# Performance work log

Measured on AMD Instinct MI355X. Metric: run time of the kernel, lower is better.

## Reference

```python
import jax, jax.numpy as jnp
import numpy as np


def setup_inputs() -> dict:
    key = jax.random.key(0)
    ks = jax.random.split(key, 5)
    B, IN, OUT = 8192, 4096, 4096
    in_q, out_q = IN // 4, OUT // 4
    # xavier-uniform-like scale for weights
    lim = float(np.sqrt(6.0 / (in_q + out_q)))
    return {
        "x": jax.random.normal(ks[0], (B, IN), dtype=jnp.float32),
        "Wa": jax.random.uniform(ks[1], (in_q, out_q), jnp.float32, -lim, lim),
        "Wb": jax.random.uniform(ks[2], (in_q, out_q), jnp.float32, -lim, lim),
        "Wc": jax.random.uniform(ks[3], (in_q, out_q), jnp.float32, -lim, lim),
        "Wd": jax.random.uniform(ks[4], (in_q, out_q), jnp.float32, -lim, lim),
        "bias": jnp.zeros((OUT,), dtype=jnp.float32),
    }


def reference(x, Wa, Wb, Wc, Wd, bias):
    # split quaternion components: [B, in_q] each
    a, b, c, d = jnp.split(x, 4, axis=1)
    # Hamilton product with weight quaternion (right multiplication)
    out_a = a @ Wa - b @ Wb - c @ Wc - d @ Wd
    out_b = a @ Wb + b @ Wa + c @ Wd - d @ Wc
    out_c = a @ Wc - b @ Wd + c @ Wa + d @ Wb
    out_d = a @ Wd + b @ Wc - c @ Wb + d @ Wa
    return jnp.concatenate([out_a, out_b, out_c, out_d], axis=1) + bias
```

## Files before the change

kernel.cpp:

```cpp
#include <hip/hip_runtime.h>
#include <hip/hip_bf16.h>
#include <cstdint>
#include <cstddef>

typedef __bf16 bf16_t;
typedef __bf16 bf16x4 __attribute__((ext_vector_type(4)));
typedef __bf16 bf16x8 __attribute__((ext_vector_type(8)));
typedef float f32x4 __attribute__((ext_vector_type(4)));

#define GLD16(src, dst)                                                       \
    __builtin_amdgcn_global_load_lds(                                         \
        (const __attribute__((address_space(1))) void*)(src),                 \
        (__attribute__((address_space(3))) void*)(dst), 16, 0, 0)

#define BAR() asm volatile("s_barrier" ::: "memory")
#define WAIT_VM4() asm volatile("s_waitcnt vmcnt(4)" ::: "memory")
#define WAIT_VM6() asm volatile("s_waitcnt vmcnt(6)" ::: "memory")
#define WAIT_VM0() asm volatile("s_waitcnt vmcnt(0)" ::: "memory")

__global__ __launch_bounds__(256) void cvt_x_kernel(const float* __restrict__ x,
                                                    bf16_t* __restrict__ xb, int n4) {
    int idx = blockIdx.x * blockDim.x + threadIdx.x;
    int stride = gridDim.x * blockDim.x;
    const f32x4* xv = (const f32x4*)x;
    bf16x4* ov = (bf16x4*)xb;
    for (int i = idx; i < n4; i += stride) {
        f32x4 v = xv[i];
        bf16x4 o;
        o[0] = (bf16_t)v[0];
        o[1] = (bf16_t)v[1];
        o[2] = (bf16_t)v[2];
        o[3] = (bf16_t)v[3];
        ov[i] = o;
    }
}

__global__ __launch_bounds__(256) void pack_w_kernel(const float* __restrict__ Wa,
                                                     const float* __restrict__ Wb,
                                                     const float* __restrict__ Wc,
                                                     const float* __restrict__ Wd,
                                                     bf16_t* __restrict__ Mt) {
    __shared__ float tile[64][65];
    const int kb = blockIdx.x * 64;
    const int nb = blockIdx.y * 64;
    const int i = kb >> 10;
    const int j = nb >> 10;

    const float* W[4] = {Wa, Wb, Wc, Wd};
    const int srcIdx[4][4] = {{0, 1, 2, 3}, {1, 0, 3, 2}, {2, 3, 0, 1}, {3, 2, 1, 0}};
    const float sgn[4][4] = {{1.f, 1.f, 1.f, 1.f},
                             {-1.f, 1.f, -1.f, 1.f},
                             {-1.f, 1.f, 1.f, -1.f},
                             {-1.f, -1.f, 1.f, 1.f}};
    const float* Ws = W[srcIdx[i][j]];
    const float s = sgn[i][j];

    const int kq = kb & 1023;
    const int nq = nb & 1023;
    const int tx = threadIdx.x & 63;
    const int ty = threadIdx.x >> 6;

    for (int r = ty; r < 64; r += 4)
        tile[r][tx] = Ws[(size_t)(kq + r) * 1024 + (nq + tx)];
    __syncthreads();
    for (int r = ty; r < 64; r += 4)
        Mt[(size_t)(nb + r) * 4096 + (kb + tx)] = (bf16_t)(s * tile[tx][r]);
}

__global__ __launch_bounds__(512, 2) void qgemm_kernel(const bf16_t* __restrict__ A,
                                                       const bf16_t* __restrict__ Bt,
                                                       const float* __restrict__ bias,
                                                       float* __restrict__ C) {
    constexpr int N = 4096, K = 4096;
    constexpr int NT = K / 64;
    extern __shared__ __align__(16) char lds[];

    const int tid = threadIdx.x;
    const int w = tid >> 6;
    const int lane = tid & 63;
    const int l15 = lane & 15, l4 = lane >> 4;
    const int wr = w >> 2, wc = w & 3;

    const int wg = blockIdx.x;
    const int swz = (wg & 7) * 64 + (wg >> 3);
    const int brow = (swz >> 4) * 256;
    const int bcol = (swz & 15) * 256;

    const int srow = lane >> 3;
    const int skb = (lane & 7) ^ (lane >> 3);

    auto stageA = [&](int buf, int h, int tt) {
#pragma unroll
        for (int q = 0; q < 2; ++q) {
            const bf16_t* src = A + (size_t)(brow + h * 128 + w * 16 + q * 8 + srow) * K +
                                tt * 64 + skb * 8;
            GLD16(src, lds + buf * 32768 + h * 16384 + w * 2048 + q * 1024);
        }
    };
    auto stageB = [&](int buf, int h, int tt) {
#pragma unroll
        for (int q = 0; q < 2; ++q) {
            const bf16_t* src = Bt + (size_t)(bcol + h * 128 + w * 16 + q * 8 + srow) * K +
                                tt * 64 + skb * 8;
            GLD16(src, lds + 65536 + buf * 32768 + h * 16384 + w * 2048 + q * 1024);
        }
    };

    f32x4 acc[8][4] = {};
    bf16x8 a[4][2], b0[2][2], b1[2][2];

    auto ldAm = [&](int buf, int mh, int m) {
#pragma unroll
        for (int c = 0; c < 2; ++c)
            a[m][c] = *(const bf16x8*)(lds + buf * 32768 + wr * 16384 +
                                       (mh * 64 + m * 16 + l15) * 128 +
                                       ((c * 4 + l4) ^ (l15 & 7)) * 16);
    };
    auto ldB = [&](int buf, int nh, bf16x8(&b)[2][2]) {
#pragma unroll
        for (int n = 0; n < 2; ++n)
#pragma unroll
            for (int c = 0; c < 2; ++c)
                b[n][c] = *(const bf16x8*)(lds + 65536 + buf * 32768 + nh * 16384 +
                                           (wc * 32 + n * 16 + l15) * 128 +
                                           ((c * 4 + l4) ^ (l15 & 7)) * 16);
    };
    auto mmac = [&](int mh, int nh, bf16x8(&b)[2][2]) {
        __builtin_amdgcn_s_setprio(1);
#pragma unroll
        for (int m = 0; m < 4; ++m)
#pragma unroll
            for (int n = 0; n < 2; ++n)
#pragma unroll
                for (int c = 0; c < 2; ++c)
                    acc[mh * 4 + m][nh * 2 + n] = __builtin_amdgcn_mfma_f32_16x16x32_bf16(
                        a[m][c], b[n][c], acc[mh * 4 + m][nh * 2 + n], 0, 0, 0);
        __builtin_amdgcn_s_setprio(0);
    };

    stageA(0, 0, 0);
    stageA(0, 1, 0);
    stageB(0, 0, 0);
    stageB(0, 1, 0);
    stageB(1, 0, 1);
    stageB(1, 1, 1);
    stageA(1, 0, 1);
    WAIT_VM6();
    BAR();
    ldB(0, 0, b0);
    ldAm(0, 0, 0);
    ldAm(0, 0, 1);

    for (int tt = 0; tt < NT; ++tt) {
        const int cur = tt & 1;
        if (tt + 1 < NT) stageA(cur ^ 1, 1, tt + 1);
        BAR();
        ldAm(cur, 0, 2);
        ldAm(cur, 0, 3);
        mmac(0, 0, b0);
        ldB(cur, 1, b1);
        BAR();
        if (tt + 2 < NT) stageB(cur, 0, tt + 2);
        BAR();
        mmac(0, 1, b1);
        ldAm(cur, 1, 0);
        ldAm(cur, 1, 1);
        BAR();
        if (tt + 2 < NT) stageB(cur, 1, tt + 2);
        BAR();
        ldAm(cur, 1, 2);
        ldAm(cur, 1, 3);
        mmac(1, 1, b1);
        if (tt + 2 < NT) {
            WAIT_VM4();
        } else {
            WAIT_VM0();
        }
        BAR();
        if (tt + 2 < NT) stageA(cur, 0, tt + 2);
        BAR();
        mmac(1, 0, b0);
        if (tt + 1 < NT) {
            ldB(cur ^ 1, 0, b0);
            ldAm(cur ^ 1, 0, 0);
            ldAm(cur ^ 1, 0, 1);
        }
        BAR();
    }

#pragma unroll
    for (int n = 0; n < 4; ++n) {
        const int col = bcol + (n >> 1) * 128 + wc * 32 + (n & 1) * 16 + l15;
        const float bv = bias[col];
#pragma unroll
        for (int m = 0; m < 8; ++m) {
            const int row0 = brow + wr * 128 + m * 16 + l4 * 4;
            const f32x4 v = acc[m][n];
#pragma unroll
            for (int i = 0; i < 4; ++i)
                C[(size_t)(row0 + i) * N + col] = v[i] + bv;
        }
    }
}

extern "C" void kernel_launch(void* const* d_in, const int* in_sizes, int n_in,
                              void* d_out, int out_size, void* d_ws, size_t ws_size,
                              hipStream_t stream) {
    const float* x = (const float*)d_in[0];
    const float* Wa = (const float*)d_in[1];
    const float* Wb = (const float*)d_in[2];
    const float* Wc = (const float*)d_in[3];
    const float* Wd = (const float*)d_in[4];
    const float* bias = (const float*)d_in[5];
    float* out = (float*)d_out;

    const int M = 8192, N = 4096, K = 4096;

    bf16_t* xb = (bf16_t*)d_ws;
    bf16_t* Mt = xb + (size_t)M * K;

    cvt_x_kernel<<<4096, 256, 0, stream>>>(x, xb, (M * K) / 4);
    pack_w_kernel<<<dim3(64, 64), 256, 0, stream>>>(Wa, Wb, Wc, Wd, Mt);

    (void)hipFuncSetAttribute((const void*)qgemm_kernel,
                              hipFuncAttributeMaxDynamicSharedMemorySize, 131072);
    qgemm_kernel<<<dim3((M / 256) * (N / 256)), 512, 131072, stream>>>(xb, Mt, bias, out);
}
```

Measured before the change: 285.2 us.

## Switch GEMM inner loop from 16x16x32 to 32x32x16 bf16 MFMA tiles

Replaces the 16x16x32 MFMA micro-tiles with 32x32x16 MFMA, reorganising the accumulators into 32x32 f32x16 blocks and the LDS fragment loads into 32-row reads across four k-slices. Larger MFMA tiles cut the number of LDS fragment reads per FLOP and give higher per-instruction throughput. In exchange it changes the register layout, the swizzled LDS read pattern and the epilogue store mapping, which may alter register pressure and LDS bank-conflict behaviour.

```diff
diff --git a/kernel.cpp b/kernel.cpp
--- a/kernel.cpp
+++ b/kernel.cpp
@@ -7,6 +7,7 @@
 typedef __bf16 bf16x4 __attribute__((ext_vector_type(4)));
 typedef __bf16 bf16x8 __attribute__((ext_vector_type(8)));
 typedef float f32x4 __attribute__((ext_vector_type(4)));
+typedef float f32x16 __attribute__((ext_vector_type(16)));
 
 #define GLD16(src, dst)                                                       \
     __builtin_amdgcn_global_load_lds(                                         \
@@ -78,7 +79,7 @@
     const int tid = threadIdx.x;
     const int w = tid >> 6;
     const int lane = tid & 63;
-    const int l15 = lane & 15, l4 = lane >> 4;
+    const int l31 = lane & 31, l5 = lane >> 5;
     const int wr = w >> 2, wc = w & 3;
 
     const int wg = blockIdx.x;
@@ -106,35 +107,34 @@
         }
     };
 
-    f32x4 acc[8][4] = {};
-    bf16x8 a[4][2], b0[2][2], b1[2][2];
-
-    auto ldAm = [&](int buf, int mh, int m) {
-#pragma unroll
-        for (int c = 0; c < 2; ++c)
-            a[m][c] = *(const bf16x8*)(lds + buf * 32768 + wr * 16384 +
-                                       (mh * 64 + m * 16 + l15) * 128 +
-                                       ((c * 4 + l4) ^ (l15 & 7)) * 16);
-    };
-    auto ldB = [&](int buf, int nh, bf16x8(&b)[2][2]) {
-#pragma unroll
-        for (int n = 0; n < 2; ++n)
-#pragma unroll
-            for (int c = 0; c < 2; ++c)
-                b[n][c] = *(const bf16x8*)(lds + 65536 + buf * 32768 + nh * 16384 +
-                                           (wc * 32 + n * 16 + l15) * 128 +
-                                           ((c * 4 + l4) ^ (l15 & 7)) * 16);
-    };
-    auto mmac = [&](int mh, int nh, bf16x8(&b)[2][2]) {
+    f32x16 acc[4][2] = {};
+    bf16x8 a[2][4];
+    bf16x8 b0[4], b1[4];
+
+    auto ldA32 = [&](int buf, int mh, int m) {
+#pragma unroll
+        for (int ks = 0; ks < 4; ++ks) {
+            const int R = mh * 64 + m * 32 + l31;
+            a[m][ks] = *(const bf16x8*)(lds + buf * 32768 + wr * 16384 + R * 128 +
+                                        (((ks * 2 + l5) ^ (R & 7)) & 7) * 16);
+        }
+    };
+    auto ldB32 = [&](int buf, int nh, bf16x8(&b)[4]) {
+#pragma unroll
+        for (int ks = 0; ks < 4; ++ks) {
+            const int R = wc * 32 + l31;
+            b[ks] = *(const bf16x8*)(lds + 65536 + buf * 32768 + nh * 16384 + R * 128 +
+                                     (((ks * 2 + l5) ^ (R & 7)) & 7) * 16);
+        }
+    };
+    auto mmac = [&](int mh, int nh, bf16x8(&b)[4]) {
         __builtin_amdgcn_s_setprio(1);
 #pragma unroll
-        for (int m = 0; m < 4; ++m)
-#pragma unroll
-            for (int n = 0; n < 2; ++n)
-#pragma unroll
-                for (int c = 0; c < 2; ++c)
-                    acc[mh * 4 + m][nh * 2 + n] = __builtin_amdgcn_mfma_f32_16x16x32_bf16(
-                        a[m][c], b[n][c], acc[mh * 4 + m][nh * 2 + n], 0, 0, 0);
+        for (int m = 0; m < 2; ++m)
+#pragma unroll
+            for (int ks = 0; ks < 4; ++ks)
+                acc[mh * 2 + m][nh] = __builtin_amdgcn_mfma_f32_32x32x16_bf16(
+                    a[m][ks], b[ks], acc[mh * 2 + m][nh], 0, 0, 0);
         __builtin_amdgcn_s_setprio(0);
     };
 
@@ -147,29 +147,25 @@
     stageA(1, 0, 1);
     WAIT_VM6();
     BAR();
-    ldB(0, 0, b0);
-    ldAm(0, 0, 0);
-    ldAm(0, 0, 1);
+    ldB32(0, 0, b0);
+    ldA32(0, 0, 0);
 
     for (int tt = 0; tt < NT; ++tt) {
         const int cur = tt & 1;
         if (tt + 1 < NT) stageA(cur ^ 1, 1, tt + 1);
         BAR();
-        ldAm(cur, 0, 2);
-        ldAm(cur, 0, 3);
+        ldA32(cur, 0, 1);
         mmac(0, 0, b0);
-        ldB(cur, 1, b1);
+        ldB32(cur, 1, b1);
         BAR();
         if (tt + 2 < NT) stageB(cur, 0, tt + 2);
         BAR();
         mmac(0, 1, b1);
-        ldAm(cur, 1, 0);
-        ldAm(cur, 1, 1);
+        ldA32(cur, 1, 0);
         BAR();
         if (tt + 2 < NT) stageB(cur, 1, tt + 2);
         BAR();
-        ldAm(cur, 1, 2);
-        ldAm(cur, 1, 3);
+        ldA32(cur, 1, 1);
         mmac(1, 1, b1);
         if (tt + 2 < NT) {
             WAIT_VM4();
@@ -181,24 +177,25 @@
         BAR();
         mmac(1, 0, b0);
         if (tt + 1 < NT) {
-            ldB(cur ^ 1, 0, b0);
-            ldAm(cur ^ 1, 0, 0);
-            ldAm(cur ^ 1, 0, 1);
+            ldB32(cur ^ 1, 0, b0);
+            ldA32(cur ^ 1, 0, 0);
         }
         BAR();
     }
 
 #pragma unroll
-    for (int n = 0; n < 4; ++n) {
-        const int col = bcol + (n >> 1) * 128 + wc * 32 + (n & 1) * 16 + l15;
+    for (int nh = 0; nh < 2; ++nh) {
+        const int col = bcol + nh * 128 + wc * 32 + l31;
         const float bv = bias[col];
 #pragma unroll
-        for (int m = 0; m < 8; ++m) {
-            const int row0 = brow + wr * 128 + m * 16 + l4 * 4;
-            const f32x4 v = acc[m][n];
-#pragma unroll
-            for (int i = 0; i < 4; ++i)
-                C[(size_t)(row0 + i) * N + col] = v[i] + bv;
+        for (int mi = 0; mi < 4; ++mi) {
+            const f32x16 v = acc[mi][nh];
+            const int row0 = brow + wr * 128 + mi * 32 + 4 * l5;
+#pragma unroll
+            for (int reg = 0; reg < 16; ++reg) {
+                const int row = row0 + (reg & 3) + 8 * (reg >> 2);
+                C[(size_t)row * N + col] = v[reg] + bv;
+            }
         }
     }
 }
```

Result: slower. 307.3 us (+7.8%).
